# Kernel optimization log

Hardware: AMD Instinct MI355X
Metric: run time of the kernel (lower is better)

Reference implementation:

```python
import jax, jax.numpy as jnp
import numpy as np

INPUT_DIM = 2048
NUM_EXPERTS = 64
TOP_K = 2


def setup_inputs() -> dict:
    key = jax.random.key(0)
    kx, kw, kb = jax.random.split(key, 3)
    x = jax.random.normal(kx, (4, 4096, INPUT_DIM), dtype=jnp.float32)
    # nn.Linear default init: U(-1/sqrt(fan_in), 1/sqrt(fan_in))
    bound = 1.0 / np.sqrt(INPUT_DIM)
    W = jax.random.uniform(kw, (INPUT_DIM, NUM_EXPERTS), dtype=jnp.float32, minval=-bound, maxval=bound)
    b = jax.random.uniform(kb, (NUM_EXPERTS,), dtype=jnp.float32, minval=-bound, maxval=bound)
    return {"x": x, "W": W, "b": b}


def reference(x, W, b):
    # dropout p=0.0 -> identity
    logits = jnp.einsum("bsd,de->bse", x, W) + b            # [B,S,E]
    topk_logits, topk_idx = jax.lax.top_k(logits, TOP_K)     # [B,S,K]
    topk_w = jax.nn.softmax(topk_logits, axis=-1)            # softmax over top-k only
    # scatter top-k weights back to full expert dim; non-top-k stay zero
    onehot = jax.nn.one_hot(topk_idx, NUM_EXPERTS, dtype=topk_w.dtype)  # [B,S,K,E]
    weights = jnp.einsum("bsk,bske->bse", topk_w, onehot)
    return weights
```

## Files before the change

kernel.cpp:

```cpp
#include <hip/hip_runtime.h>
#include <math.h>

#define D 2048
#define E 64
#define TOK 64
#define THREADS 256
#define NKC 4
#define KCH (D / NKC)
#define SK 16
#define NSTEP (KCH / SK)

typedef float4 f4;

__device__ __forceinline__ float fget(const float4 v, int j) {
    return j == 0 ? v.x : j == 1 ? v.y : j == 2 ? v.z : v.w;
}

__device__ __forceinline__ void fmablock(float (&acc)[8][8],
                                         const float4 (&xw)[2],
                                         const float4 (&ww)[2]) {
#pragma unroll
    for (int t = 0; t < 8; ++t) {
        const float xt = fget(t < 4 ? xw[0] : xw[1], t & 3);
#pragma unroll
        for (int e = 0; e < 8; ++e) {
            const float we = fget(e < 4 ? ww[0] : ww[1], e & 3);
            acc[t][e] = fmaf(xt, we, acc[t][e]);
        }
    }
}

__device__ __forceinline__ void tile_store(float* b, const float (&acc)[8][8],
                                           int tg, int eg) {
#pragma unroll
    for (int t = 0; t < 8; ++t) {
        f4 v0 = {acc[t][0], acc[t][1], acc[t][2], acc[t][3]};
        f4 v1 = {acc[t][4], acc[t][5], acc[t][6], acc[t][7]};
        *(f4*)(b + (tg * 8 + t) * 65 + eg * 8) = v0;
        *(f4*)(b + (tg * 8 + t) * 65 + eg * 8 + 4) = v1;
    }
}

__device__ __forceinline__ void tile_addin(const float* b, float (&acc)[8][8],
                                           int tg, int eg) {
#pragma unroll
    for (int t = 0; t < 8; ++t) {
        f4 v0 = *(const f4*)(b + (tg * 8 + t) * 65 + eg * 8);
        f4 v1 = *(const f4*)(b + (tg * 8 + t) * 65 + eg * 8 + 4);
        acc[t][0] += v0.x; acc[t][1] += v0.y; acc[t][2] += v0.z; acc[t][3] += v0.w;
        acc[t][4] += v1.x; acc[t][5] += v1.y; acc[t][6] += v1.z; acc[t][7] += v1.w;
    }
}

__global__ __launch_bounds__(THREADS)
void gating_kernel(const float* __restrict__ x,
                   const float* __restrict__ W,
                   const float* __restrict__ Bv,
                   float* __restrict__ out)
{
    __shared__ __align__(16) float smem[16384];

    const int tid  = threadIdx.x;
    const int lane = tid & 63;
    const int w    = __builtin_amdgcn_readfirstlane(tid >> 6);
    const int tg   = lane >> 3;
    const int eg   = lane & 7;
    const int tok0 = blockIdx.x * TOK;

    float* base  = smem + w * 4096;
    float* xbuf0 = base;
    float* xbuf1 = base + 1024;
    float* wbuf0 = base + 2048;
    float* wbuf1 = base + 3072;

    const float* xg = x + (size_t)(tok0 + lane) * D + w * KCH;
    const float* wg = W + (size_t)w * KCH * E;
    const int wr = lane >> 2, wq = lane & 3;

    float acc[8][8];
#pragma unroll
    for (int t = 0; t < 8; ++t)
#pragma unroll
        for (int e = 0; e < 8; ++e) acc[t][e] = 0.f;

    float4 xs[4], ws[4];
#pragma unroll
    for (int c = 0; c < 4; ++c) xs[c] = *(const f4*)(xg + c * 4);
#pragma unroll
    for (int c = 0; c < 4; ++c)
        ws[c] = *(const f4*)(wg + (size_t)wr * E + (wq + c * 4) * 4);
#pragma unroll
    for (int j = 0; j < 16; ++j) xbuf0[j * 64 + lane] = fget(xs[j >> 2], j & 3);
#pragma unroll
    for (int c = 0; c < 4; ++c)
        *(f4*)(wbuf0 + wr * 64 + (wq + c * 4) * 4) = ws[c];
#pragma unroll
    for (int c = 0; c < 4; ++c) xs[c] = *(const f4*)(xg + SK + c * 4);
#pragma unroll
    for (int c = 0; c < 4; ++c)
        ws[c] = *(const f4*)(wg + (size_t)(SK + wr) * E + (wq + c * 4) * 4);

    float4 xw[2][2], ww[2][2];
    xw[0][0] = *(const f4*)(xbuf0 + tg * 8);
    xw[0][1] = *(const f4*)(xbuf0 + tg * 8 + 4);
    ww[0][0] = *(const f4*)(wbuf0 + eg * 8);
    ww[0][1] = *(const f4*)(wbuf0 + eg * 8 + 4);
    xw[1][0] = *(const f4*)(xbuf0 + 64 + tg * 8);
    xw[1][1] = *(const f4*)(xbuf0 + 64 + tg * 8 + 4);
    ww[1][0] = *(const f4*)(wbuf0 + 64 + eg * 8);
    ww[1][1] = *(const f4*)(wbuf0 + 64 + eg * 8 + 4);

#pragma unroll 1
    for (int s = 0; s < NSTEP; ++s) {
        float* xc = (s & 1) ? xbuf1 : xbuf0;
        float* wc = (s & 1) ? wbuf1 : wbuf0;
        float* xn = (s & 1) ? xbuf0 : xbuf1;
        float* wn = (s & 1) ? wbuf0 : wbuf1;
        if (s < NSTEP - 1) {
#pragma unroll
            for (int j = 0; j < 16; ++j) xn[j * 64 + lane] = fget(xs[j >> 2], j & 3);
#pragma unroll
            for (int c = 0; c < 4; ++c)
                *(f4*)(wn + wr * 64 + (wq + c * 4) * 4) = ws[c];
            const int s2 = (s + 2 < NSTEP) ? s + 2 : NSTEP - 1;
#pragma unroll
            for (int c = 0; c < 4; ++c)
                xs[c] = *(const f4*)(xg + s2 * SK + c * 4);
#pragma unroll
            for (int c = 0; c < 4; ++c)
                ws[c] = *(const f4*)(wg + (size_t)(s2 * SK + wr) * E + (wq + c * 4) * 4);
        }
        const float* xnx = (s < NSTEP - 1) ? xn : xc;
        const float* wnx = (s < NSTEP - 1) ? wn : wc;
#pragma unroll
        for (int r = 0; r < 16; ++r) {
            const int p = r & 1;
            fmablock(acc, xw[p], ww[p]);
            const float* xsrc = (r < 14) ? (xc + (r + 2) * 64) : (xnx + (r - 14) * 64);
            const float* wsrc = (r < 14) ? (wc + (r + 2) * 64) : (wnx + (r - 14) * 64);
            xw[p][0] = *(const f4*)(xsrc + tg * 8);
            xw[p][1] = *(const f4*)(xsrc + tg * 8 + 4);
            ww[p][0] = *(const f4*)(wsrc + eg * 8);
            ww[p][1] = *(const f4*)(wsrc + eg * 8 + 4);
        }
    }

    float* buf0 = smem;
    float* buf1 = smem + 4160;
    __syncthreads();
    if (w == 2) tile_store(buf0, acc, tg, eg);
    if (w == 3) tile_store(buf1, acc, tg, eg);
    __syncthreads();
    if (w == 0) tile_addin(buf0, acc, tg, eg);
    if (w == 1) tile_addin(buf1, acc, tg, eg);
    __syncthreads();
    if (w == 1) tile_store(buf0, acc, tg, eg);
    __syncthreads();
    if (w == 0) {
        tile_addin(buf0, acc, tg, eg);
        tile_store(buf0, acc, tg, eg);
    }
    __syncthreads();

    float* logits = buf0;
    float* sw1 = smem + 8320; float* sw2 = smem + 8384;
    int*   si1 = (int*)(smem + 8448); int* si2 = (int*)(smem + 8512);

    if (w == 0) {
        float m1 = -3.4e38f, m2 = -3.4e38f;
        int i1 = 0, i2 = 0;
#pragma unroll
        for (int e = 0; e < E; ++e) {
            float v = logits[lane * 65 + e] + Bv[e];
            if (v > m1)      { m2 = m1; i2 = i1; m1 = v; i1 = e; }
            else if (v > m2) { m2 = v; i2 = e; }
        }
        float p = 1.0f / (1.0f + expf(m2 - m1));
        sw1[lane] = p; sw2[lane] = 1.0f - p;
        si1[lane] = i1; si2[lane] = i2;
    }
    __syncthreads();

    float4* o4 = (float4*)(out + (size_t)tok0 * E);
#pragma unroll
    for (int p5 = 0; p5 < 4; ++p5) {
        int idx = tid + p5 * 256;
        int tl  = idx >> 4;
        int e0  = (idx & 15) * 4;
        int a1 = si1[tl], a2 = si2[tl];
        float v1 = sw1[tl], v2 = sw2[tl];
        float4 v;
        v.x = (e0 + 0 == a1) ? v1 : (e0 + 0 == a2) ? v2 : 0.0f;
        v.y = (e0 + 1 == a1) ? v1 : (e0 + 1 == a2) ? v2 : 0.0f;
        v.z = (e0 + 2 == a1) ? v1 : (e0 + 2 == a2) ? v2 : 0.0f;
        v.w = (e0 + 3 == a1) ? v1 : (e0 + 3 == a2) ? v2 : 0.0f;
        o4[idx] = v;
    }
}

extern "C" void kernel_launch(void* const* d_in, const int* in_sizes, int n_in,
                              void* d_out, int out_size, void* d_ws, size_t ws_size,
                              hipStream_t stream) {
    const float* x = (const float*)d_in[0];
    const float* W = (const float*)d_in[1];
    const float* b = (const float*)d_in[2];
    float* out = (float*)d_out;

    const int tokens = in_sizes[0] / D;
    const int blocks = tokens / TOK;

    gating_kernel<<<blocks, THREADS, 0, stream>>>(x, W, b, out);
}
```

Before: 251.6 us.

## Split K across 16 waves per block with tree reduction of partial tiles

Raises the block to 1024 threads and splits the 2048-long reduction into 16 chunks, one per wave, with a smaller k-step of 8. Partial 64x64 logit tiles are combined by a four-level tree reduction through shared memory, and W staging now uses coalesced scalar loads. The aim is more in-flight memory parallelism and latency hiding per block. In exchange the kernel needs 128KB of shared memory, which limits resident blocks per CU, and adds extra barriers and reduction traffic.

```diff
diff --git a/kernel.cpp b/kernel.cpp
--- a/kernel.cpp
+++ b/kernel.cpp
@@ -4,10 +4,10 @@
 #define D 2048
 #define E 64
 #define TOK 64
-#define THREADS 256
-#define NKC 4
+#define THREADS 1024
+#define NKC 16
 #define KCH (D / NKC)
-#define SK 16
+#define SK 8
 #define NSTEP (KCH / SK)
 
 typedef float4 f4;
@@ -36,8 +36,8 @@
     for (int t = 0; t < 8; ++t) {
         f4 v0 = {acc[t][0], acc[t][1], acc[t][2], acc[t][3]};
         f4 v1 = {acc[t][4], acc[t][5], acc[t][6], acc[t][7]};
-        *(f4*)(b + (tg * 8 + t) * 65 + eg * 8) = v0;
-        *(f4*)(b + (tg * 8 + t) * 65 + eg * 8 + 4) = v1;
+        *(f4*)(b + (tg * 8 + t) * 64 + eg * 8) = v0;
+        *(f4*)(b + (tg * 8 + t) * 64 + eg * 8 + 4) = v1;
     }
 }
 
@@ -45,8 +45,8 @@
                                            int tg, int eg) {
 #pragma unroll
     for (int t = 0; t < 8; ++t) {
-        f4 v0 = *(const f4*)(b + (tg * 8 + t) * 65 + eg * 8);
-        f4 v1 = *(const f4*)(b + (tg * 8 + t) * 65 + eg * 8 + 4);
+        f4 v0 = *(const f4*)(b + (tg * 8 + t) * 64 + eg * 8);
+        f4 v1 = *(const f4*)(b + (tg * 8 + t) * 64 + eg * 8 + 4);
         acc[t][0] += v0.x; acc[t][1] += v0.y; acc[t][2] += v0.z; acc[t][3] += v0.w;
         acc[t][4] += v1.x; acc[t][5] += v1.y; acc[t][6] += v1.z; acc[t][7] += v1.w;
     }
@@ -58,7 +58,7 @@
                    const float* __restrict__ Bv,
                    float* __restrict__ out)
 {
-    __shared__ __align__(16) float smem[16384];
+    __shared__ __align__(16) float smem[32768];
 
     const int tid  = threadIdx.x;
     const int lane = tid & 63;
@@ -67,15 +67,14 @@
     const int eg   = lane & 7;
     const int tok0 = blockIdx.x * TOK;
 
-    float* base  = smem + w * 4096;
+    float* base  = smem + w * 2048;
     float* xbuf0 = base;
-    float* xbuf1 = base + 1024;
-    float* wbuf0 = base + 2048;
-    float* wbuf1 = base + 3072;
+    float* xbuf1 = base + 512;
+    float* wbuf0 = base + 1024;
+    float* wbuf1 = base + 1536;
 
     const float* xg = x + (size_t)(tok0 + lane) * D + w * KCH;
     const float* wg = W + (size_t)w * KCH * E;
-    const int wr = lane >> 2, wq = lane & 3;
 
     float acc[8][8];
 #pragma unroll
@@ -83,22 +82,20 @@
 #pragma unroll
         for (int e = 0; e < 8; ++e) acc[t][e] = 0.f;
 
-    float4 xs[4], ws[4];
-#pragma unroll
-    for (int c = 0; c < 4; ++c) xs[c] = *(const f4*)(xg + c * 4);
-#pragma unroll
-    for (int c = 0; c < 4; ++c)
-        ws[c] = *(const f4*)(wg + (size_t)wr * E + (wq + c * 4) * 4);
-#pragma unroll
-    for (int j = 0; j < 16; ++j) xbuf0[j * 64 + lane] = fget(xs[j >> 2], j & 3);
-#pragma unroll
-    for (int c = 0; c < 4; ++c)
-        *(f4*)(wbuf0 + wr * 64 + (wq + c * 4) * 4) = ws[c];
-#pragma unroll
-    for (int c = 0; c < 4; ++c) xs[c] = *(const f4*)(xg + SK + c * 4);
-#pragma unroll
-    for (int c = 0; c < 4; ++c)
-        ws[c] = *(const f4*)(wg + (size_t)(SK + wr) * E + (wq + c * 4) * 4);
+    float4 xs[2];
+    float  ws[8];
+    xs[0] = *(const f4*)(xg);
+    xs[1] = *(const f4*)(xg + 4);
+#pragma unroll
+    for (int j = 0; j < 8; ++j) ws[j] = wg[j * E + lane];
+#pragma unroll
+    for (int j = 0; j < 8; ++j) xbuf0[j * 64 + lane] = fget(xs[j >> 2], j & 3);
+#pragma unroll
+    for (int j = 0; j < 8; ++j) wbuf0[j * 64 + lane] = ws[j];
+    xs[0] = *(const f4*)(xg + SK);
+    xs[1] = *(const f4*)(xg + SK + 4);
+#pragma unroll
+    for (int j = 0; j < 8; ++j) ws[j] = wg[(SK + j) * E + lane];
 
     float4 xw[2][2], ww[2][2];
     xw[0][0] = *(const f4*)(xbuf0 + tg * 8);
@@ -118,26 +115,25 @@
         float* wn = (s & 1) ? wbuf0 : wbuf1;
         if (s < NSTEP - 1) {
 #pragma unroll
-            for (int j = 0; j < 16; ++j) xn[j * 64 + lane] = fget(xs[j >> 2], j & 3);
-#pragma unroll
-            for (int c = 0; c < 4; ++c)
-                *(f4*)(wn + wr * 64 + (wq + c * 4) * 4) = ws[c];
+            for (int j = 0; j < 8; ++j) xn[j * 64 + lane] = fget(xs[j >> 2], j & 3);
+#pragma unroll
+            for (int j = 0; j < 8; ++j) wn[j * 64 + lane] = ws[j];
             const int s2 = (s + 2 < NSTEP) ? s + 2 : NSTEP - 1;
-#pragma unroll
-            for (int c = 0; c < 4; ++c)
-                xs[c] = *(const f4*)(xg + s2 * SK + c * 4);
-#pragma unroll
-            for (int c = 0; c < 4; ++c)
-                ws[c] = *(const f4*)(wg + (size_t)(s2 * SK + wr) * E + (wq + c * 4) * 4);
+            xs[0] = *(const f4*)(xg + s2 * SK);
+            xs[1] = *(const f4*)(xg + s2 * SK + 4);
+#pragma unroll
+            for (int j = 0; j < 8; ++j) ws[j] = wg[(s2 * SK + j) * E + lane];
         }
         const float* xnx = (s < NSTEP - 1) ? xn : xc;
         const float* wnx = (s < NSTEP - 1) ? wn : wc;
 #pragma unroll
-        for (int r = 0; r < 16; ++r) {
+        for (int r = 0; r < SK; ++r) {
             const int p = r & 1;
             fmablock(acc, xw[p], ww[p]);
-            const float* xsrc = (r < 14) ? (xc + (r + 2) * 64) : (xnx + (r - 14) * 64);
-            const float* wsrc = (r < 14) ? (wc + (r + 2) * 64) : (wnx + (r - 14) * 64);
+            const float* xsrc = (r < SK - 2) ? (xc + (r + 2) * 64)
+                                             : (xnx + (r - (SK - 2)) * 64);
+            const float* wsrc = (r < SK - 2) ? (wc + (r + 2) * 64)
+                                             : (wnx + (r - (SK - 2)) * 64);
             xw[p][0] = *(const f4*)(xsrc + tg * 8);
             xw[p][1] = *(const f4*)(xsrc + tg * 8 + 4);
             ww[p][0] = *(const f4*)(wsrc + eg * 8);
@@ -145,26 +141,35 @@
         }
     }
 
-    float* buf0 = smem;
-    float* buf1 = smem + 4160;
-    __syncthreads();
-    if (w == 2) tile_store(buf0, acc, tg, eg);
-    if (w == 3) tile_store(buf1, acc, tg, eg);
-    __syncthreads();
-    if (w == 0) tile_addin(buf0, acc, tg, eg);
-    if (w == 1) tile_addin(buf1, acc, tg, eg);
-    __syncthreads();
-    if (w == 1) tile_store(buf0, acc, tg, eg);
-    __syncthreads();
+    __syncthreads();
+    if (w >= 8) tile_store(smem + (w - 8) * 4096, acc, tg, eg);
+    __syncthreads();
+    if (w < 8)  tile_addin(smem + w * 4096, acc, tg, eg);
+    __syncthreads();
+    if (w >= 4 && w < 8) tile_store(smem + (w - 4) * 4096, acc, tg, eg);
+    __syncthreads();
+    if (w < 4)  tile_addin(smem + w * 4096, acc, tg, eg);
+    __syncthreads();
+    if (w == 2 || w == 3) tile_store(smem + (w - 2) * 4096, acc, tg, eg);
+    __syncthreads();
+    if (w < 2)  tile_addin(smem + w * 4096, acc, tg, eg);
+    __syncthreads();
+    if (w == 1) tile_store(smem, acc, tg, eg);
+    __syncthreads();
+
+    float* logits = smem + 4096;
+    float* sw1 = smem + 8704; float* sw2 = smem + 8768;
+    int*   si1 = (int*)(smem + 8832); int* si2 = (int*)(smem + 8896);
+
     if (w == 0) {
-        tile_addin(buf0, acc, tg, eg);
-        tile_store(buf0, acc, tg, eg);
-    }
-    __syncthreads();
-
-    float* logits = buf0;
-    float* sw1 = smem + 8320; float* sw2 = smem + 8384;
-    int*   si1 = (int*)(smem + 8448); int* si2 = (int*)(smem + 8512);
+        tile_addin(smem, acc, tg, eg);
+#pragma unroll
+        for (int t = 0; t < 8; ++t)
+#pragma unroll
+            for (int e = 0; e < 8; ++e)
+                logits[(tg * 8 + t) * 65 + eg * 8 + e] = acc[t][e];
+    }
+    __syncthreads();
 
     if (w == 0) {
         float m1 = -3.4e38f, m2 = -3.4e38f;
@@ -182,9 +187,8 @@
     __syncthreads();
 
     float4* o4 = (float4*)(out + (size_t)tok0 * E);
-#pragma unroll
-    for (int p5 = 0; p5 < 4; ++p5) {
-        int idx = tid + p5 * 256;
+    {
+        int idx = tid;
         int tl  = idx >> 4;
         int e0  = (idx & 15) * 4;
         int a1 = si1[tl], a2 = si2[tl];
```

After: 406.9 us. 1.62x slower.
